# Performance work log

Hardware: AMD Instinct MI355X
Metric: run time of the kernel (lower is better)

## Reference

```python
import jax, jax.numpy as jnp
import numpy as np

B, L = 16, 512          # samples x tokens-per-sample
S = B * L               # total packed tokens
H, HKV, D = 16, 4, 128  # query heads, kv heads, head_dim
G = H // HKV            # GQA group size
HID = 2048
EPS = 1e-6


def rmsnorm(x, w):
    # Qwen2RMSNorm: fp32 variance, scale by weight
    v = jnp.mean(x.astype(jnp.float32) ** 2, axis=-1, keepdims=True)
    return (x.astype(jnp.float32) * jax.lax.rsqrt(v + EPS)).astype(x.dtype) * w


def rotate_half(x):
    x1, x2 = jnp.split(x, 2, axis=-1)
    return jnp.concatenate([-x2, x1], axis=-1)


def setup_inputs() -> dict:
    key = jax.random.key(0)
    ks = jax.random.split(key, 24)
    f = lambda k, shp, s=0.02: (jax.random.normal(k, shp, dtype=jnp.float32) * s)
    inp = {
        'packed_sequence_und': f(ks[0], (S // 2, HID), 1.0),
        'packed_sequence_gen': f(ks[1], (S // 2, HID), 1.0),
        # und tokens on even slots, gen on odd slots -> irregular scatter
        'packed_und_token_indexes': jnp.arange(0, S, 2, dtype=jnp.int32),
        'packed_gen_token_indexes': jnp.arange(1, S, 2, dtype=jnp.int32),
        # und-path projections (q/k/v have bias, o does not)
        'q_w': f(ks[2], (H * D, HID)), 'q_b': f(ks[3], (H * D,)),
        'k_w': f(ks[4], (HKV * D, HID)), 'k_b': f(ks[5], (HKV * D,)),
        'v_w': f(ks[6], (HKV * D, HID)), 'v_b': f(ks[7], (HKV * D,)),
        'o_w': f(ks[8], (HID, H * D)),
        # gen-path (moe_gen) projections
        'q_w_g': f(ks[9], (H * D, HID)), 'q_b_g': f(ks[10], (H * D,)),
        'k_w_g': f(ks[11], (HKV * D, HID)), 'k_b_g': f(ks[12], (HKV * D,)),
        'v_w_g': f(ks[13], (HKV * D, HID)), 'v_b_g': f(ks[14], (HKV * D,)),
        'o_w_g': f(ks[15], (HID, H * D)),
        # qk-norm weights
        'qn_w': jnp.ones((D,), jnp.float32), 'kn_w': jnp.ones((D,), jnp.float32),
        'qn_w_g': jnp.ones((D,), jnp.float32), 'kn_w_g': jnp.ones((D,), jnp.float32),
    }
    # RoPE cos/sin for packed positions (position resets per sample)
    pos = jnp.tile(jnp.arange(L, dtype=jnp.float32), B)            # [S]
    inv_freq = 1.0 / (1e6 ** (jnp.arange(0, D, 2, dtype=jnp.float32) / D))
    freqs = pos[:, None] * inv_freq[None, :]                       # [S, D/2]
    emb = jnp.concatenate([freqs, freqs], axis=-1)                 # [S, D]
    inp['packed_cos'] = jnp.cos(emb)
    inp['packed_sin'] = jnp.sin(emb)
    return inp


def reference(packed_sequence_und, packed_sequence_gen, packed_cos, packed_sin,
              packed_und_token_indexes, packed_gen_token_indexes,
              q_w, q_b, k_w, k_b, v_w, v_b, o_w,
              q_w_g, q_b_g, k_w_g, k_b_g, v_w_g, v_b_g, o_w_g,
              qn_w, kn_w, qn_w_g, kn_w_g):
    ui, gi = packed_und_token_indexes, packed_gen_token_indexes
    # dual-path QKV projection + index scatter into shared packed buffers
    q = jnp.zeros((S, H * D), jnp.float32)
    q = q.at[ui].set(packed_sequence_und @ q_w.T + q_b)
    q = q.at[gi].set(packed_sequence_gen @ q_w_g.T + q_b_g)
    k = jnp.zeros((S, HKV * D), jnp.float32)
    k = k.at[ui].set(packed_sequence_und @ k_w.T + k_b)
    k = k.at[gi].set(packed_sequence_gen @ k_w_g.T + k_b_g)
    v = jnp.zeros((S, HKV * D), jnp.float32)
    v = v.at[ui].set(packed_sequence_und @ v_w.T + v_b)
    v = v.at[gi].set(packed_sequence_gen @ v_w_g.T + v_b_g)

    q = q.reshape(S, H, D)
    k = k.reshape(S, HKV, D)
    v = v.reshape(S, HKV, D)

    # per-stream QK RMSNorm, scattered back
    q = jnp.zeros_like(q).at[ui].set(rmsnorm(q[ui], qn_w)).at[gi].set(rmsnorm(q[gi], qn_w_g))
    k = jnp.zeros_like(k).at[ui].set(rmsnorm(k[ui], kn_w)).at[gi].set(rmsnorm(k[gi], kn_w_g))

    # RoPE (unsqueeze_dim=1)
    cos, sin = packed_cos[:, None, :], packed_sin[:, None, :]
    q = q * cos + rotate_half(q) * sin
    k = k * cos + rotate_half(k) * sin

    # block-diagonal causal attention over packed samples (GQA)
    qb_ = q.reshape(B, L, HKV, G, D)
    kb_ = k.reshape(B, L, HKV, D)
    vb_ = v.reshape(B, L, HKV, D)
    scale = 1.0 / np.sqrt(D)
    scores = jnp.einsum('bqhgd,bkhd->bhgqk', qb_, kb_) * scale   # [B,HKV,G,L,L]
    causal = jnp.tril(jnp.ones((L, L), bool))
    scores = jnp.where(causal, scores, -jnp.inf)
    probs = jax.nn.softmax(scores, axis=-1)
    out = jnp.einsum('bhgqk,bkhd->bqhgd', probs, vb_)            # [B,L,HKV,G,D]
    out = out.reshape(S, H * D)

    out_und = out[ui] @ o_w.T
    out_gen = out[gi] @ o_w_g.T
    return (out_und, out_gen)
```

## Files before the change

### kernel.cpp

```cpp
#include <hip/hip_runtime.h>

typedef __bf16 bf16;
typedef __bf16 bf16x8 __attribute__((ext_vector_type(8)));
typedef float  f32x4  __attribute__((ext_vector_type(4)));

#define HALF   4096
#define S_TOT  8192
#define HID    2048
#define NH     16
#define NKV    4
#define DH     128
#define LSEQ   512

typedef const __attribute__((address_space(1))) void* as1_cvp;
typedef __attribute__((address_space(3))) void* as3_vp;

__device__ __forceinline__ void gl2lds16(const void* g, void* l) {
    __builtin_amdgcn_global_load_lds((as1_cvp)g, (as3_vp)l, 16, 0, 0);
}

__device__ __forceinline__ void hard_barrier() {
    __builtin_amdgcn_sched_barrier(0);
    __builtin_amdgcn_s_barrier();
    __builtin_amdgcn_sched_barrier(0);
}
#define VMCNT(n) asm volatile("s_waitcnt vmcnt(" #n ")" ::: "memory")

struct CvtArgs {
    const float* src[10];
    bf16*        dst[10];
    int          n4[10];
};
__global__ __launch_bounds__(256) void k_convert_multi(CvtArgs a, int total4) {
    int i = blockIdx.x * 256 + threadIdx.x;
    if (i >= total4) return;
    int off = i;
    #pragma unroll
    for (int s = 0; s < 10; ++s) {
        if (off < a.n4[s]) {
            float4 v = ((const float4*)a.src[s])[off];
            union { bf16 b[4]; ushort4 u; } t;
            t.b[0] = (bf16)v.x; t.b[1] = (bf16)v.y; t.b[2] = (bf16)v.z; t.b[3] = (bf16)v.w;
            ((ushort4*)a.dst[s])[off] = t.u;
            return;
        }
        off -= a.n4[s];
    }
}

__global__ void k_invtyp(const int* __restrict__ ui, const int* __restrict__ gi,
                         int* __restrict__ it) {
    int t = blockIdx.x * 256 + threadIdx.x;
    if (t < HALF) { it[ui[t]] = t << 1; it[gi[t]] = (t << 1) | 1; }
}

__device__ __forceinline__ void stage_chunk(const bf16* __restrict__ g,
    int row0, int kcol, char* chunk, int tid)
{
    const int wave = tid >> 6;
    #pragma unroll
    for (int j = 0; j < 2; ++j) {
        const int sidx = j*512 + tid;
        const int row  = sidx >> 2;
        const int csw  = (sidx & 3) ^ ((row >> 1) & 3);
        gl2lds16(g + (size_t)(row0 + row)*HID + kcol + csw*8,
                 chunk + (size_t)(j*512 + wave*64)*16);
    }
}

#define PHASE(BUF, MH, KH, STG, TAIL)                                           \
  {                                                                             \
    const char* Ab_ = sAb + (BUF)*32768 + (KH)*16384;                           \
    const char* Bb_ = sBb + (BUF)*32768 + (KH)*16384;                           \
    bf16x8 af_[4], bf_[4];                                                      \
    _Pragma("unroll")                                                           \
    for (int im = 0; im < 4; ++im)                                              \
        af_[im] = *(const bf16x8*)(Ab_ + aoff[MH][im]);                         \
    _Pragma("unroll")                                                           \
    for (int jn = 0; jn < 4; ++jn)                                              \
        bf_[jn] = *(const bf16x8*)(Bb_ + boff[jn]);                             \
    STG;                                                                        \
    hard_barrier();                                                             \
    __builtin_amdgcn_s_setprio(1);                                              \
    _Pragma("unroll")                                                           \
    for (int im = 0; im < 4; ++im)                                              \
      _Pragma("unroll")                                                         \
      for (int jn = 0; jn < 4; ++jn)                                            \
        acc[(MH)*4+im][jn] = __builtin_amdgcn_mfma_f32_16x16x32_bf16(           \
            af_[im], bf_[jn], acc[(MH)*4+im][jn], 0, 0, 0);                     \
    __builtin_amdgcn_s_setprio(0);                                              \
    TAIL;                                                                       \
    hard_barrier();                                                             \
  }

__device__ __forceinline__ void gemm256_core(
    const bf16* __restrict__ A, const bf16* __restrict__ B,
    int m0, int n0, int tid, char* sAb, char* sBb, f32x4 (&acc)[8][4])
{
    const int lane = tid & 63;
    const int lm = lane & 15, kq = lane >> 4;
    const int wave = tid >> 6;
    const int wm = wave >> 2, wn = wave & 3;

    int aoff[2][4]; int boff[4];
    #pragma unroll
    for (int mh = 0; mh < 2; ++mh)
        #pragma unroll
        for (int im = 0; im < 4; ++im) {
            const int row = wm*128 + mh*64 + im*16 + lm;
            aoff[mh][im] = row*64 + ((kq ^ ((row >> 1) & 3)) * 16);
        }
    #pragma unroll
    for (int jn = 0; jn < 4; ++jn) {
        const int row = wn*64 + jn*16 + lm;
        boff[jn] = row*64 + ((kq ^ ((row >> 1) & 3)) * 16);
    }

    stage_chunk(A, m0, 0,  sAb + 0,     tid);
    stage_chunk(A, m0, 32, sAb + 16384, tid);
    stage_chunk(B, n0, 0,  sBb + 0,     tid);
    stage_chunk(B, n0, 32, sBb + 16384, tid);
    stage_chunk(A, m0, 64, sAb + 32768, tid);
    stage_chunk(B, n0, 64, sBb + 32768, tid);
    VMCNT(4);
    hard_barrier();

    #pragma unroll 1
    for (int i = 0; i < 15; ++i) {
        const int t1k = (2*i+1)*64, t2k = (2*i+2)*64, t3k = (2*i+3)*64;
        PHASE(0,0,0, stage_chunk(A, m0, t1k+32, sAb + 49152, tid), (void)0);
        PHASE(0,1,0, stage_chunk(B, n0, t1k+32, sBb + 49152, tid), (void)0);
        PHASE(0,0,1, stage_chunk(A, m0, t2k,    sAb + 0,     tid), (void)0);
        PHASE(0,1,1, stage_chunk(B, n0, t2k,    sBb + 0,     tid), VMCNT(4));
        PHASE(1,0,0, stage_chunk(A, m0, t2k+32, sAb + 16384, tid), (void)0);
        PHASE(1,1,0, stage_chunk(B, n0, t2k+32, sBb + 16384, tid), (void)0);
        PHASE(1,0,1, stage_chunk(A, m0, t3k,    sAb + 32768, tid), (void)0);
        PHASE(1,1,1, stage_chunk(B, n0, t3k,    sBb + 32768, tid), VMCNT(4));
    }
    {
        PHASE(0,0,0, stage_chunk(A, m0, 2016, sAb + 49152, tid), (void)0);
        PHASE(0,1,0, stage_chunk(B, n0, 2016, sBb + 49152, tid), (void)0);
        PHASE(0,0,1, (void)0, (void)0);
        PHASE(0,1,1, (void)0, VMCNT(0));
        PHASE(1,0,0, (void)0, (void)0);
        PHASE(1,1,0, (void)0, (void)0);
        PHASE(1,0,1, (void)0, (void)0);
        PHASE(1,1,1, (void)0, (void)0);
    }
}

__global__ __launch_bounds__(512, 2) void k_gemm_qkv(
    const bf16* __restrict__ Xu, const bf16* __restrict__ Xg,
    const bf16* __restrict__ Wu, const bf16* __restrict__ Wg,
    const float* __restrict__ qbu, const float* __restrict__ kbu, const float* __restrict__ vbu,
    const float* __restrict__ qbg, const float* __restrict__ kbg, const float* __restrict__ vbg,
    const int* __restrict__ ui, const int* __restrict__ gi,
    bf16* __restrict__ qo, bf16* __restrict__ ko, bf16* __restrict__ vo)
{
    __shared__ __align__(16) bf16 sA[2][2][256*32];
    __shared__ __align__(16) bf16 sB[2][2][256*32];

    const int gen = blockIdx.z;
    const bf16* X = gen ? Xg : Xu;
    const bf16* W = gen ? Wg : Wu;
    const float* qb = gen ? qbg : qbu;
    const float* kb = gen ? kbg : kbu;
    const float* vb = gen ? vbg : vbu;
    const int* idx = gen ? gi : ui;

    const int tid = threadIdx.x;
    const int wave = tid >> 6, lane = tid & 63;
    const int lm = lane & 15, kq = lane >> 4;
    const int wm = wave >> 2, wn = wave & 3;
    const int m0 = blockIdx.y * 256, n0 = blockIdx.x * 256;

    f32x4 acc[8][4] = {};
    gemm256_core(X, W, m0, n0, tid, (char*)&sA[0][0][0], (char*)&sB[0][0][0], acc);

    #pragma unroll
    for (int im = 0; im < 8; ++im) {
        int srow[4];
        #pragma unroll
        for (int r = 0; r < 4; ++r) srow[r] = idx[m0 + wm*128 + im*16 + kq*4 + r];
        #pragma unroll
        for (int jn = 0; jn < 4; ++jn) {
            const int o = n0 + wn*64 + jn*16 + lm;
            bf16* dst; float bias; int off0, ld;
            if (o < 2048)      { dst = qo; ld = 2048; off0 = o;        bias = qb[o]; }
            else if (o < 2560) { dst = ko; ld = 512;  off0 = o - 2048; bias = kb[o-2048]; }
            else               { dst = vo; ld = 512;  off0 = o - 2560; bias = vb[o-2560]; }
            #pragma unroll
            for (int r = 0; r < 4; ++r)
                dst[(size_t)srow[r]*ld + off0] = (bf16)(acc[im][jn][r] + bias);
        }
    }
}

__global__ __launch_bounds__(256) void k_norm_rope(
    bf16* __restrict__ qbuf, bf16* __restrict__ kbuf,
    const float* __restrict__ cosb, const float* __restrict__ sinb,
    const int* __restrict__ invtyp,
    const float* __restrict__ qnu, const float* __restrict__ qng,
    const float* __restrict__ knu, const float* __restrict__ kng)
{
    const int row = blockIdx.x * 4 + (threadIdx.x >> 6);
    const int lane = threadIdx.x & 63;
    const int s = row / (NH + NKV), hh = row % (NH + NKV);
    const int isg = invtyp[s] & 1;
    bf16* ptr; const float* w; float qs;
    if (hh < NH) { ptr = qbuf + (size_t)s*HID + hh*DH;           w = isg ? qng : qnu;
                   qs = 0.08838834764831845f * 1.4426950408889634f; }
    else         { ptr = kbuf + (size_t)s*(NKV*DH) + (hh-NH)*DH; w = isg ? kng : knu;
                   qs = 1.0f; }

    const unsigned u = *(const unsigned*)((const unsigned short*)ptr + 2*lane);
    const float f0 = __uint_as_float(u << 16);
    const float f1 = __uint_as_float(u & 0xffff0000u);
    float ss = f0*f0 + f1*f1;
    #pragma unroll
    for (int m = 32; m; m >>= 1) ss += __shfl_xor(ss, m, 64);
    const float r = rsqrtf(ss * (1.0f/128.0f) + 1e-6f);
    const float2 wv = *(const float2*)(w + 2*lane);
    const float xn0 = f0 * r * wv.x;
    const float xn1 = f1 * r * wv.y;
    const float po0 = __shfl_xor(xn0, 32, 64);
    const float po1 = __shfl_xor(xn1, 32, 64);
    const float2 c2 = *(const float2*)(cosb + (size_t)s*DH + 2*lane);
    const float2 s2 = *(const float2*)(sinb + (size_t)s*DH + 2*lane);
    const float sg = (lane < 32) ? -1.0f : 1.0f;
    const float o0 = (xn0 * c2.x + sg * po0 * s2.x) * qs;
    const float o1 = (xn1 * c2.y + sg * po1 * s2.y) * qs;
    union { unsigned short us[2]; unsigned u; } t;
    bf16 b0 = (bf16)o0, b1 = (bf16)o1;
    t.us[0] = *(unsigned short*)&b0; t.us[1] = *(unsigned short*)&b1;
    *(unsigned*)((unsigned short*)ptr + 2*lane) = t.u;
}

__global__ __launch_bounds__(256) void k_vtrans(const bf16* __restrict__ v, bf16* __restrict__ vt)
{
    __shared__ __align__(16) bf16 sT[64 * 132];
    const int kvh = blockIdx.y;
    const int s0 = blockIdx.x * 64;
    const int b = s0 >> 9;
    const int pos0 = s0 & 511;
    const int tid = threadIdx.x;

    #pragma unroll
    for (int i = 0; i < 4; ++i) {
        const int c = i*256 + tid;
        const int rowi = c >> 4, col8 = c & 15;
        const uint4 d = *(const uint4*)(v + (size_t)(s0 + rowi)*(NKV*DH) + kvh*DH + col8*8);
        uint2* lp = (uint2*)&sT[rowi*132 + col8*8];
        lp[0] = make_uint2(d.x, d.y);
        lp[1] = make_uint2(d.z, d.w);
    }
    __syncthreads();
    const int dd = tid >> 1, half = tid & 1;
    __align__(16) bf16 tmp[32];
    #pragma unroll
    for (int p = 0; p < 32; ++p) tmp[p] = sT[(half*32 + p)*132 + dd];
    bf16* dst = vt + ((size_t)(b*NKV + kvh)*DH + dd)*LSEQ + pos0 + half*32;
    #pragma unroll
    for (int q = 0; q < 8; ++q) ((ushort4*)dst)[q] = ((ushort4*)tmp)[q];
}

__global__ __launch_bounds__(256) void k_attn(
    const bf16* __restrict__ qbuf, const bf16* __restrict__ kbuf,
    const bf16* __restrict__ vt, const int* __restrict__ invtyp,
    bf16* __restrict__ aop_u, bf16* __restrict__ aop_g)
{
    __shared__ __align__(16) bf16 sK[2][64*128];
    __shared__ __align__(16) bf16 sV[2][128*64];
    __shared__ __align__(16) bf16 sP[4][16*72];

    const int qt = 7 - blockIdx.x;
    const int h = blockIdx.y, b = blockIdx.z;
    const int kvh = h >> 2;
    const int tid = threadIdx.x, wave = tid >> 6, lane = tid & 63;
    const int lm = lane & 15, kq = lane >> 4;
    const int q0 = qt * 64;

    bf16x8 qfrag[4];
    {
        const bf16* qp = qbuf + ((size_t)(b*LSEQ + q0 + wave*16 + lm))*HID + h*DH;
        #pragma unroll
        for (int ks = 0; ks < 4; ++ks)
            qfrag[ks] = *(const bf16x8*)(qp + ks*32 + kq*8);
    }

    const bf16* kbase = kbuf + ((size_t)(b*LSEQ))*(NKV*DH) + kvh*DH;
    const bf16* vbase = vt + ((size_t)(b*NKV + kvh)*DH)*LSEQ;

    f32x4 accO[8] = {};
    float lpart[4] = {0.f, 0.f, 0.f, 0.f};
    bf16* const sPw = &sP[wave][0];

    {
        const bf16* kp = kbase;
        const bf16* vp = vbase;
        #pragma unroll
        for (int i = 0; i < 4; ++i) {
            const int g = i*4 + wave;
            const int ch = g*64 + lane;
            { const int row = ch >> 4, cp = ch & 15;
              const int c = (cp & 8) | ((cp ^ row) & 7);
              gl2lds16(kp + (size_t)row*(NKV*DH) + c*8, (char*)&sK[0][0] + (size_t)g*1024); }
            { const int d = ch >> 3, cp = ch & 7;
              const int c = (cp ^ d) & 7;
              gl2lds16(vp + (size_t)d*LSEQ + c*8, (char*)&sV[0][0] + (size_t)g*1024); }
        }
    }

    for (int kt = 0; kt <= qt; ++kt) {
        const int cur = kt & 1;
        __syncthreads();

        if (kt < qt) {
            const bf16* kp = kbase + (size_t)((kt+1)*64)*(NKV*DH);
            const bf16* vp = vbase + (kt+1)*64;
            const int nxt = cur ^ 1;
            #pragma unroll
            for (int i = 0; i < 4; ++i) {
                const int g = i*4 + wave;
                const int ch = g*64 + lane;
                { const int row = ch >> 4, cp = ch & 15;
                  const int c = (cp & 8) | ((cp ^ row) & 7);
                  gl2lds16(kp + (size_t)row*(NKV*DH) + c*8, (char*)&sK[nxt][0] + (size_t)g*1024); }
                { const int d = ch >> 3, cp = ch & 7;
                  const int c = (cp ^ d) & 7;
                  gl2lds16(vp + (size_t)d*LSEQ + c*8, (char*)&sV[nxt][0] + (size_t)g*1024); }
            }
        }

        f32x4 s4[4] = {};
        #pragma unroll
        for (int ks = 0; ks < 4; ++ks) {
            const int cq = ks*4 + kq;
            const int cs = (cq & 8) | ((cq ^ lm) & 7);
            #pragma unroll
            for (int nt = 0; nt < 4; ++nt) {
                bf16x8 bk = *(const bf16x8*)&sK[cur][(nt*16 + lm)*128 + cs*8];
                s4[nt] = __builtin_amdgcn_mfma_f32_16x16x32_bf16(qfrag[ks], bk, s4[nt], 0, 0, 0);
            }
        }

        const bool diag = (kt == qt);
        #pragma unroll
        for (int r = 0; r < 4; ++r) {
            const int rloc = wave*16 + kq*4 + r;
            float v0 = s4[0][r], v1 = s4[1][r], v2 = s4[2][r], v3 = s4[3][r];
            if (diag) {
                if (lm      > rloc) v0 = -1e30f;
                if (lm + 16 > rloc) v1 = -1e30f;
                if (lm + 32 > rloc) v2 = -1e30f;
                if (lm + 48 > rloc) v3 = -1e30f;
            }
            const float p0 = exp2f(v0);
            const float p1 = exp2f(v1);
            const float p2 = exp2f(v2);
            const float p3 = exp2f(v3);
            lpart[r] += (p0 + p1) + (p2 + p3);
            const int prow = (kq*4 + r) * 72;
            sPw[prow + lm]      = (bf16)p0;
            sPw[prow + 16 + lm] = (bf16)p1;
            sPw[prow + 32 + lm] = (bf16)p2;
            sPw[prow + 48 + lm] = (bf16)p3;
        }

        #pragma unroll
        for (int pc = 0; pc < 2; ++pc) {
            bf16x8 ap = *(const bf16x8*)&sPw[lm*72 + pc*32 + kq*8];
            #pragma unroll
            for (int dt = 0; dt < 8; ++dt) {
                const int cv = (pc*4 + kq);
                const int cs = (cv ^ lm) & 7;
                bf16x8 bv = *(const bf16x8*)&sV[cur][(dt*16 + lm)*64 + cs*8];
                accO[dt] = __builtin_amdgcn_mfma_f32_16x16x32_bf16(ap, bv, accO[dt], 0, 0, 0);
            }
        }
    }

    #pragma unroll
    for (int r = 0; r < 4; ++r) {
        float l = lpart[r];
        l += __shfl_xor(l, 1, 64);
        l += __shfl_xor(l, 2, 64);
        l += __shfl_xor(l, 4, 64);
        l += __shfl_xor(l, 8, 64);
        const int srow = b*LSEQ + q0 + wave*16 + kq*4 + r;
        const int code = invtyp[srow];
        bf16* dst = (code & 1) ? aop_g : aop_u;
        const size_t off = (size_t)(code >> 1)*HID + h*DH;
        const float inv_l = 1.0f / l;
        #pragma unroll
        for (int dt = 0; dt < 8; ++dt)
            dst[off + dt*16 + lm] = (bf16)(accO[dt][r] * inv_l);
    }
}

__global__ __launch_bounds__(512, 2) void k_gemm_out(
    const bf16* __restrict__ Au, const bf16* __restrict__ Ag,
    const bf16* __restrict__ Wu, const bf16* __restrict__ Wg,
    float* __restrict__ out)
{
    __shared__ __align__(16) bf16 sA[2][2][256*32];
    __shared__ __align__(16) bf16 sB[2][2][256*32];

    const int gen = blockIdx.z;
    const bf16* A = gen ? Ag : Au;
    const bf16* W = gen ? Wg : Wu;
    float* O = out + (size_t)gen * HALF * HID;

    const int tid = threadIdx.x;
    const int wave = tid >> 6, lane = tid & 63;
    const int lm = lane & 15, kq = lane >> 4;
    const int wm = wave >> 2, wn = wave & 3;
    const int m0 = blockIdx.y * 256, n0 = blockIdx.x * 256;

    f32x4 acc[8][4] = {};
    gemm256_core(A, W, m0, n0, tid, (char*)&sA[0][0][0], (char*)&sB[0][0][0], acc);

    #pragma unroll
    for (int im = 0; im < 8; ++im)
        #pragma unroll
        for (int jn = 0; jn < 4; ++jn)
            #pragma unroll
            for (int r = 0; r < 4; ++r)
                O[(size_t)(m0 + wm*128 + im*16 + kq*4 + r)*HID + (n0 + wn*64 + jn*16 + lm)]
                    = acc[im][jn][r];
}

extern "C" void kernel_launch(void* const* d_in, const int* in_sizes, int n_in,
                              void* d_out, int out_size, void* d_ws, size_t ws_size,
                              hipStream_t stream)
{
    (void)in_sizes; (void)n_in; (void)out_size; (void)ws_size;
    const float* x_u  = (const float*)d_in[0];
    const float* x_g  = (const float*)d_in[1];
    const int*   ui   = (const int*)d_in[2];
    const int*   gi   = (const int*)d_in[3];
    const float* q_w  = (const float*)d_in[4];
    const float* q_b  = (const float*)d_in[5];
    const float* k_w  = (const float*)d_in[6];
    const float* k_b  = (const float*)d_in[7];
    const float* v_w  = (const float*)d_in[8];
    const float* v_b  = (const float*)d_in[9];
    const float* o_w  = (const float*)d_in[10];
    const float* q_wg = (const float*)d_in[11];
    const float* q_bg = (const float*)d_in[12];
    const float* k_wg = (const float*)d_in[13];
    const float* k_bg = (const float*)d_in[14];
    const float* v_wg = (const float*)d_in[15];
    const float* v_bg = (const float*)d_in[16];
    const float* o_wg = (const float*)d_in[17];
    const float* qn_u = (const float*)d_in[18];
    const float* kn_u = (const float*)d_in[19];
    const float* qn_g = (const float*)d_in[20];
    const float* kn_g = (const float*)d_in[21];
    const float* cosb = (const float*)d_in[22];
    const float* sinb = (const float*)d_in[23];

    char* w = (char*)d_ws;
    auto alloc = [&](size_t bytes) { char* p = w; w += (bytes + 255) & ~(size_t)255; return p; };
    bf16* xb_u   = (bf16*)alloc((size_t)HALF*HID*2);
    bf16* xb_g   = (bf16*)alloc((size_t)HALF*HID*2);
    bf16* wqkv_u = (bf16*)alloc((size_t)3072*HID*2);
    bf16* wqkv_g = (bf16*)alloc((size_t)3072*HID*2);
    bf16* wo_u   = (bf16*)alloc((size_t)HID*HID*2);
    bf16* wo_g   = (bf16*)alloc((size_t)HID*HID*2);
    bf16* qbuf   = (bf16*)alloc((size_t)S_TOT*HID*2);
    bf16* kbuf   = (bf16*)alloc((size_t)S_TOT*NKV*DH*2);
    bf16* vbuf   = (bf16*)alloc((size_t)S_TOT*NKV*DH*2);
    bf16* vtb    = (bf16*)alloc((size_t)S_TOT*NKV*DH*2);
    int*  invtyp = (int*)alloc((size_t)S_TOT*4);
    bf16* aop_u = xb_u;
    bf16* aop_g = xb_g;

    CvtArgs ca;
    int total4 = 0, si = 0;
    auto seg = [&](const float* s, bf16* d, size_t n) {
        ca.src[si] = s; ca.dst[si] = d; ca.n4[si] = (int)(n / 4);
        total4 += (int)(n / 4); ++si;
    };
    seg(x_u,  xb_u,                (size_t)HALF*HID);
    seg(x_g,  xb_g,                (size_t)HALF*HID);
    seg(q_w,  wqkv_u,              (size_t)2048*HID);
    seg(k_w,  wqkv_u + 2048*HID,   (size_t)512*HID);
    seg(v_w,  wqkv_u + 2560*HID,   (size_t)512*HID);
    seg(q_wg, wqkv_g,              (size_t)2048*HID);
    seg(k_wg, wqkv_g + 2048*HID,   (size_t)512*HID);
    seg(v_wg, wqkv_g + 2560*HID,   (size_t)512*HID);
    seg(o_w,  wo_u,                (size_t)HID*HID);
    seg(o_wg, wo_g,                (size_t)HID*HID);
    k_convert_multi<<<(total4 + 255)/256, 256, 0, stream>>>(ca, total4);

    k_invtyp<<<16, 256, 0, stream>>>(ui, gi, invtyp);

    k_gemm_qkv<<<dim3(12, 16, 2), 512, 0, stream>>>(
        xb_u, xb_g, wqkv_u, wqkv_g,
        q_b, k_b, v_b, q_bg, k_bg, v_bg,
        ui, gi, qbuf, kbuf, vbuf);

    k_norm_rope<<<(S_TOT*(NH+NKV))/4, 256, 0, stream>>>(
        qbuf, kbuf, cosb, sinb, invtyp, qn_u, qn_g, kn_u, kn_g);

    k_vtrans<<<dim3(S_TOT/64, NKV), 256, 0, stream>>>(vbuf, vtb);

    k_attn<<<dim3(LSEQ/64, NH, 16), 256, 0, stream>>>(
        qbuf, kbuf, vtb, invtyp, aop_u, aop_g);

    k_gemm_out<<<dim3(8, 16, 2), 512, 0, stream>>>(
        aop_u, aop_g, wo_u, wo_g, (float*)d_out);
}
```

Baseline: 542.7 us.

## Prefetch next LDS fragments into ping-pong registers and drop mid-phase barrier

Restructures the 256x256 GEMM main loop so each phase loads the next phase's A/B fragments from LDS into alternate register sets while the MFMAs use the current ones. This removes one of the two barriers per phase and overlaps LDS reads with matrix math. Address computation is also simplified into precomputed base offsets and global offsets. The cost is more vector registers and changed wait counts, which risks races or register spills at 2 waves/SIMD occupancy.

```diff
diff --git a/kernel.cpp b/kernel.cpp
--- a/kernel.cpp
+++ b/kernel.cpp
@@ -54,40 +54,28 @@
     if (t < HALF) { it[ui[t]] = t << 1; it[gi[t]] = (t << 1) | 1; }
 }
 
-__device__ __forceinline__ void stage_chunk(const bf16* __restrict__ g,
-    int row0, int kcol, char* chunk, int tid)
-{
-    const int wave = tid >> 6;
-    #pragma unroll
-    for (int j = 0; j < 2; ++j) {
-        const int sidx = j*512 + tid;
-        const int row  = sidx >> 2;
-        const int csw  = (sidx & 3) ^ ((row >> 1) & 3);
-        gl2lds16(g + (size_t)(row0 + row)*HID + kcol + csw*8,
-                 chunk + (size_t)(j*512 + wave*64)*16);
-    }
-}
-
-#define PHASE(BUF, MH, KH, STG, TAIL)                                           \
+#define STG2(MB, KC, DST)                                                       \
+    gl2lds16((MB) + (KC) + go0, (DST) + wave*1024);                             \
+    gl2lds16((MB) + (KC) + go1, (DST) + 8192 + wave*1024);
+
+#define GPHASE(UA, UB, RA, RB, DO_B, NOFF, NMH, MH, STG, TAIL)                  \
   {                                                                             \
-    const char* Ab_ = sAb + (BUF)*32768 + (KH)*16384;                           \
-    const char* Bb_ = sBb + (BUF)*32768 + (KH)*16384;                           \
-    bf16x8 af_[4], bf_[4];                                                      \
     _Pragma("unroll")                                                           \
     for (int im = 0; im < 4; ++im)                                              \
-        af_[im] = *(const bf16x8*)(Ab_ + aoff[MH][im]);                         \
-    _Pragma("unroll")                                                           \
-    for (int jn = 0; jn < 4; ++jn)                                              \
-        bf_[jn] = *(const bf16x8*)(Bb_ + boff[jn]);                             \
+        RA[im] = *(const bf16x8*)(sAb + (NOFF) + (NMH)*4096 + im*1024 + abase); \
+    if (DO_B) {                                                                 \
+        _Pragma("unroll")                                                       \
+        for (int jn = 0; jn < 4; ++jn)                                          \
+            RB[jn] = *(const bf16x8*)(sBb + (NOFF) + jn*1024 + bbase);          \
+    }                                                                           \
     STG;                                                                        \
-    hard_barrier();                                                             \
     __builtin_amdgcn_s_setprio(1);                                              \
     _Pragma("unroll")                                                           \
     for (int im = 0; im < 4; ++im)                                              \
       _Pragma("unroll")                                                         \
       for (int jn = 0; jn < 4; ++jn)                                            \
         acc[(MH)*4+im][jn] = __builtin_amdgcn_mfma_f32_16x16x32_bf16(           \
-            af_[im], bf_[jn], acc[(MH)*4+im][jn], 0, 0, 0);                     \
+            UA[im], UB[jn], acc[(MH)*4+im][jn], 0, 0, 0);                       \
     __builtin_amdgcn_s_setprio(0);                                              \
     TAIL;                                                                       \
     hard_barrier();                                                             \
@@ -102,50 +90,53 @@
     const int wave = tid >> 6;
     const int wm = wave >> 2, wn = wave & 3;
 
-    int aoff[2][4]; int boff[4];
-    #pragma unroll
-    for (int mh = 0; mh < 2; ++mh)
-        #pragma unroll
-        for (int im = 0; im < 4; ++im) {
-            const int row = wm*128 + mh*64 + im*16 + lm;
-            aoff[mh][im] = row*64 + ((kq ^ ((row >> 1) & 3)) * 16);
-        }
-    #pragma unroll
-    for (int jn = 0; jn < 4; ++jn) {
-        const int row = wn*64 + jn*16 + lm;
-        boff[jn] = row*64 + ((kq ^ ((row >> 1) & 3)) * 16);
-    }
-
-    stage_chunk(A, m0, 0,  sAb + 0,     tid);
-    stage_chunk(A, m0, 32, sAb + 16384, tid);
-    stage_chunk(B, n0, 0,  sBb + 0,     tid);
-    stage_chunk(B, n0, 32, sBb + 16384, tid);
-    stage_chunk(A, m0, 64, sAb + 32768, tid);
-    stage_chunk(B, n0, 64, sBb + 32768, tid);
+    const int swz16 = (kq ^ ((lm >> 1) & 3)) * 16;
+    const int abase = wm*8192 + lm*64 + swz16;
+    const int bbase = wn*4096 + lm*64 + swz16;
+
+    int go0, go1;
+    {
+        const int s0 = tid,        r0 = s0 >> 2, c0 = (s0 & 3) ^ ((r0 >> 1) & 3);
+        const int s1 = 512 + tid,  r1 = s1 >> 2, c1 = (s1 & 3) ^ ((r1 >> 1) & 3);
+        go0 = r0*HID + c0*8;
+        go1 = r1*HID + c1*8;
+    }
+    const bf16* Ab = A + (size_t)m0*HID;
+    const bf16* Bb = B + (size_t)n0*HID;
+
+    bf16x8 afA[4], afB[4], bfA[4], bfB[4];
+
+    STG2(Ab, 0,  sAb + 0);      STG2(Ab, 32, sAb + 16384);
+    STG2(Bb, 0,  sBb + 0);      STG2(Bb, 32, sBb + 16384);
+    STG2(Ab, 64, sAb + 32768);  STG2(Bb, 64, sBb + 32768);
     VMCNT(4);
     hard_barrier();
+    #pragma unroll
+    for (int im = 0; im < 4; ++im) afA[im] = *(const bf16x8*)(sAb + im*1024 + abase);
+    #pragma unroll
+    for (int jn = 0; jn < 4; ++jn) bfA[jn] = *(const bf16x8*)(sBb + jn*1024 + bbase);
 
     #pragma unroll 1
     for (int i = 0; i < 15; ++i) {
-        const int t1k = (2*i+1)*64, t2k = (2*i+2)*64, t3k = (2*i+3)*64;
-        PHASE(0,0,0, stage_chunk(A, m0, t1k+32, sAb + 49152, tid), (void)0);
-        PHASE(0,1,0, stage_chunk(B, n0, t1k+32, sBb + 49152, tid), (void)0);
-        PHASE(0,0,1, stage_chunk(A, m0, t2k,    sAb + 0,     tid), (void)0);
-        PHASE(0,1,1, stage_chunk(B, n0, t2k,    sBb + 0,     tid), VMCNT(4));
-        PHASE(1,0,0, stage_chunk(A, m0, t2k+32, sAb + 16384, tid), (void)0);
-        PHASE(1,1,0, stage_chunk(B, n0, t2k+32, sBb + 16384, tid), (void)0);
-        PHASE(1,0,1, stage_chunk(A, m0, t3k,    sAb + 32768, tid), (void)0);
-        PHASE(1,1,1, stage_chunk(B, n0, t3k,    sBb + 32768, tid), VMCNT(4));
+        const int kc = 128*i;
+        GPHASE(afA,bfA, afB,bfA, 0, 0,     1, 0, STG2(Ab, kc+96,  sAb+49152), VMCNT(6));
+        GPHASE(afB,bfA, afA,bfB, 1, 16384, 0, 1, STG2(Bb, kc+96,  sBb+49152), (void)0);
+        GPHASE(afA,bfB, afB,bfA, 0, 16384, 1, 0, STG2(Ab, kc+128, sAb+0),     VMCNT(6));
+        GPHASE(afB,bfB, afA,bfA, 1, 32768, 0, 1, STG2(Bb, kc+128, sBb+0),     (void)0);
+        GPHASE(afA,bfA, afB,bfA, 0, 32768, 1, 0, STG2(Ab, kc+160, sAb+16384), VMCNT(6));
+        GPHASE(afB,bfA, afA,bfB, 1, 49152, 0, 1, STG2(Bb, kc+160, sBb+16384), (void)0);
+        GPHASE(afA,bfB, afB,bfA, 0, 49152, 1, 0, STG2(Ab, kc+192, sAb+32768), VMCNT(6));
+        GPHASE(afB,bfB, afA,bfA, 1, 0,     0, 1, STG2(Bb, kc+192, sBb+32768), (void)0);
     }
     {
-        PHASE(0,0,0, stage_chunk(A, m0, 2016, sAb + 49152, tid), (void)0);
-        PHASE(0,1,0, stage_chunk(B, n0, 2016, sBb + 49152, tid), (void)0);
-        PHASE(0,0,1, (void)0, (void)0);
-        PHASE(0,1,1, (void)0, VMCNT(0));
-        PHASE(1,0,0, (void)0, (void)0);
-        PHASE(1,1,0, (void)0, (void)0);
-        PHASE(1,0,1, (void)0, (void)0);
-        PHASE(1,1,1, (void)0, (void)0);
+        GPHASE(afA,bfA, afB,bfA, 0, 0,     1, 0, STG2(Ab, 2016, sAb+49152), VMCNT(6));
+        GPHASE(afB,bfA, afA,bfB, 1, 16384, 0, 1, STG2(Bb, 2016, sBb+49152), (void)0);
+        GPHASE(afA,bfB, afB,bfA, 0, 16384, 1, 0, (void)0,                   VMCNT(4));
+        GPHASE(afB,bfB, afA,bfA, 1, 32768, 0, 1, (void)0,                   (void)0);
+        GPHASE(afA,bfA, afB,bfA, 0, 32768, 1, 0, (void)0,                   VMCNT(0));
+        GPHASE(afB,bfA, afA,bfB, 1, 49152, 0, 1, (void)0,                   (void)0);
+        GPHASE(afA,bfB, afB,bfA, 0, 49152, 1, 0, (void)0,                   (void)0);
+        GPHASE(afB,bfB, afA,bfA, 1, 0,     0, 1, (void)0,                   (void)0);
     }
 }
 
```

Result: no change. 540.9 us (-0.3%).
